# Kernel tuning notes

Measured on AMD Instinct MI355X. Metric: run time of the kernel, lower is better.

Reference implementation:

```python
import jax, jax.numpy as jnp
import numpy as np

N_EXPERTS = 8
TOP_K = 2

def setup_inputs() -> dict:
    key = jax.random.key(0)
    k1, k2, k3, k4 = jax.random.split(key, 4)
    B, T, C, F, E = 4, 1024, 1024, 2048, N_EXPERTS
    x = jax.random.normal(k1, (B, T, C), dtype=jnp.float32)
    router_w = jax.random.normal(k2, (E, C), dtype=jnp.float32) * 0.02
    w_v = jax.random.normal(k3, (E, C, 2 * F), dtype=jnp.float32) * 0.02
    c_proj = jax.random.normal(k4, (E, F, C), dtype=jnp.float32) * 0.02
    return {"x": x, "router_w": router_w, "w_v": w_v, "c_proj": c_proj}

def reference(x, router_w, w_v, c_proj):
    B, T, C = x.shape
    E = router_w.shape[0]
    # Router: top-k softmax
    logits = jnp.einsum('btc,ec->bte', x, router_w)
    probs = jax.nn.softmax(logits, axis=-1)
    weights, indices = jax.lax.top_k(probs, TOP_K)          # [B,T,K]
    weights = weights / jnp.sum(weights, axis=-1, keepdims=True)
    avg_probs = jnp.mean(probs, axis=(0, 1))
    aux_loss = E * jnp.sum(avg_probs * avg_probs)
    # Dense per-expert SwiGLU MLP on all tokens (idiomatic jax MoE reference)
    xf = x.reshape(B * T, C)                                # [N,C]
    h = jnp.einsum('nc,ecf->enf', xf, w_v)                  # [E,N,2F]
    gate, value = jnp.split(h, 2, axis=-1)
    act = jax.nn.silu(gate) * value                         # [E,N,F]
    eo = jnp.einsum('enf,efc->nec', act, c_proj)            # [N,E,C]
    # Combine: gather each token's top-k expert outputs and weight-sum
    idx = indices.reshape(B * T, TOP_K)                     # [N,K]
    w = weights.reshape(B * T, TOP_K)                       # [N,K]
    sel = jnp.take_along_axis(eo, idx[:, :, None], axis=1)  # [N,K,C]
    out = jnp.sum(w[:, :, None] * sel, axis=1)              # [N,C]
    return out.reshape(B, T, C), aux_loss
```

## Files before the change

kernel.cpp:

```cpp
#include <hip/hip_runtime.h>
#include <hip/hip_bf16.h>
#include <stdint.h>

#define N_TOK 4096
#define C_DIM 1024
#define F_DIM 2048
#define E_NUM 8
#define SMAX 9216
#define TILES_MAX 72
#define RBLK 1024

typedef __attribute__((ext_vector_type(4))) float f32x4;
typedef __attribute__((ext_vector_type(8))) short s16x8;

__device__ __forceinline__ uint16_t f2bf(float f) {
    unsigned x;
    __builtin_memcpy(&x, &f, 4);
    unsigned r = (x + 0x7fffu + ((x >> 16) & 1u)) >> 16;
    return (uint16_t)r;
}
__device__ __forceinline__ float bf2f(uint16_t u) {
    unsigned v = (unsigned)u << 16;
    float f;
    __builtin_memcpy(&f, &v, 4);
    return f;
}

#define GLL16(gp, lp)                                                                  \
    __builtin_amdgcn_global_load_lds((const __attribute__((address_space(1))) unsigned int*)(gp), \
                                     (__attribute__((address_space(3))) unsigned int*)(lp), 16, 0, 0)

__global__ void router_kernel(const float* __restrict__ x, const float* __restrict__ rw,
                              int* __restrict__ topk_idx, float* __restrict__ topk_w,
                              float* __restrict__ psum_part, int* __restrict__ cnt_part) {
    __shared__ float s_p[E_NUM];
    __shared__ int s_c[E_NUM];
    if (threadIdx.x < E_NUM) { s_p[threadIdx.x] = 0.f; s_c[threadIdx.x] = 0; }
    __syncthreads();

    int lane = threadIdx.x & 63;
    int wv = threadIdx.x >> 6;
    int t = blockIdx.x * 4 + wv;

    const float* xr = x + (size_t)t * C_DIM + lane * 16;
    float xs[16];
    for (int i = 0; i < 4; i++) *(float4*)&xs[i * 4] = *(const float4*)(xr + i * 4);

    float acc[E_NUM];
    for (int e = 0; e < E_NUM; e++) {
        const float* wr = rw + e * C_DIM + lane * 16;
        float s = 0.f;
        for (int i = 0; i < 4; i++) {
            float4 v = *(const float4*)(wr + i * 4);
            s += xs[i * 4] * v.x + xs[i * 4 + 1] * v.y + xs[i * 4 + 2] * v.z + xs[i * 4 + 3] * v.w;
        }
        acc[e] = s;
    }
    for (int off = 32; off > 0; off >>= 1)
        for (int e = 0; e < E_NUM; e++) acc[e] += __shfl_down(acc[e], off, 64);

    if (lane == 0) {
        float m = acc[0];
        for (int e = 1; e < E_NUM; e++) m = fmaxf(m, acc[e]);
        float p[E_NUM], s = 0.f;
        for (int e = 0; e < E_NUM; e++) { p[e] = __expf(acc[e] - m); s += p[e]; }
        float inv = 1.f / s;
        for (int e = 0; e < E_NUM; e++) { p[e] *= inv; atomicAdd(&s_p[e], p[e]); }
        int i0 = 0;
        for (int e = 1; e < E_NUM; e++) if (p[e] > p[i0]) i0 = e;
        int i1 = (i0 == 0) ? 1 : 0;
        for (int e = 0; e < E_NUM; e++) if (e != i0 && p[e] > p[i1]) i1 = e;
        float w0 = p[i0], w1 = p[i1], wsum = w0 + w1;
        topk_idx[t * 2] = i0; topk_idx[t * 2 + 1] = i1;
        topk_w[t * 2] = w0 / wsum; topk_w[t * 2 + 1] = w1 / wsum;
        atomicAdd(&s_c[i0], 1); atomicAdd(&s_c[i1], 1);
    }
    __syncthreads();
    if (threadIdx.x < E_NUM) {
        psum_part[blockIdx.x * E_NUM + threadIdx.x] = s_p[threadIdx.x];
        cnt_part[blockIdx.x * E_NUM + threadIdx.x] = s_c[threadIdx.x];
    }
}

__global__ void reduce_plan_kernel(const float* __restrict__ psum_part, const int* __restrict__ cnt_part,
                                   int* __restrict__ offsets, int* __restrict__ tile_expert,
                                   int* __restrict__ tile_row0, float* __restrict__ aux_out) {
    __shared__ float sp[256];
    __shared__ int sc[256];
    __shared__ int s_count[E_NUM];
    __shared__ float s_psum[E_NUM];
    int e = threadIdx.x >> 5, i = threadIdx.x & 31;
    float fp = 0.f; int c = 0;
    for (int j = i; j < RBLK; j += 32) { fp += psum_part[j * E_NUM + e]; c += cnt_part[j * E_NUM + e]; }
    sp[threadIdx.x] = fp; sc[threadIdx.x] = c;
    __syncthreads();
    for (int s = 16; s > 0; s >>= 1) {
        if (i < s) { sp[threadIdx.x] += sp[threadIdx.x + s]; sc[threadIdx.x] += sc[threadIdx.x + s]; }
        __syncthreads();
    }
    if (i == 0) { s_count[e] = sc[threadIdx.x]; s_psum[e] = sp[threadIdx.x]; }
    __syncthreads();
    if (threadIdx.x == 0) {
        int off = 0, t = 0;
        for (int ee = 0; ee < E_NUM; ee++) {
            offsets[ee] = off;
            int n = s_count[ee];
            int nt = (n + 127) >> 7;
            for (int k = 0; k < nt; k++) { tile_expert[t] = ee; tile_row0[t] = off + k * 128; t++; }
            off += nt * 128;
        }
        offsets[E_NUM] = off;
        for (; t < TILES_MAX; t++) tile_expert[t] = -1;
        float s = 0.f;
        for (int ee = 0; ee < E_NUM; ee++) { float a = s_psum[ee] * (1.f / N_TOK); s += a * a; }
        aux_out[0] = 8.f * s;
    }
}

__global__ void assign_kernel(const int* __restrict__ topk_idx, const float* __restrict__ topk_w,
                              const int* __restrict__ offsets, int* __restrict__ count2,
                              int* __restrict__ slot_map, float* __restrict__ slot_w,
                              int* __restrict__ tok_slot) {
    __shared__ int h[E_NUM];
    __shared__ int base[E_NUM];
    if (threadIdx.x < E_NUM) h[threadIdx.x] = 0;
    __syncthreads();
    int item = blockIdx.x * 256 + threadIdx.x;
    int e = topk_idx[item];
    int rank = atomicAdd(&h[e], 1);
    __syncthreads();
    if (threadIdx.x < E_NUM)
        base[threadIdx.x] = offsets[threadIdx.x] + atomicAdd(&count2[threadIdx.x], h[threadIdx.x]);
    __syncthreads();
    int slot = base[e] + rank;
    slot_map[slot] = item;
    slot_w[slot] = topk_w[item];
    tok_slot[item] = slot;
}

__global__ void gather_kernel(const float* __restrict__ x, const int* __restrict__ slot_map,
                              uint16_t* __restrict__ x_slots) {
    int slot = blockIdx.x;
    int item = slot_map[slot];
    if (item < 0) return;
    int t = item >> 1;
    float4 v = *(const float4*)(x + (size_t)t * C_DIM + threadIdx.x * 4);
    union { uint16_t u[4]; uint2 q; } r;
    r.u[0] = f2bf(v.x); r.u[1] = f2bf(v.y); r.u[2] = f2bf(v.z); r.u[3] = f2bf(v.w);
    *(uint2*)(x_slots + (size_t)slot * C_DIM + threadIdx.x * 4) = r.q;
}

__global__ __launch_bounds__(256) void convT_both(const float* __restrict__ wv, uint16_t* __restrict__ wvT,
                                                  const float* __restrict__ cp, uint16_t* __restrict__ cpT) {
    __shared__ uint16_t s[128 * 66];
    int bid = blockIdx.x;
    const float* in; uint16_t* out; int R, Cc, bx, by, bz;
    if (bid < 4096) {
        in = wv; out = wvT; R = 1024; Cc = 4096;
        bx = bid & 63; by = (bid >> 6) & 7; bz = bid >> 9;
    } else {
        int b = bid - 4096;
        in = cp; out = cpT; R = 2048; Cc = 1024;
        bx = b & 15; by = (b >> 4) & 15; bz = b >> 8;
    }
    size_t zb = (size_t)bz * (size_t)R * Cc;
    int c0 = bx * 64, r0 = by * 128;
    int cx = (threadIdx.x & 15) * 4, ry = threadIdx.x >> 4;
    for (int j = 0; j < 8; j++) {
        int r = ry + j * 16;
        float4 v = *(const float4*)(in + zb + (size_t)(r0 + r) * Cc + c0 + cx);
        uint16_t* p = &s[r * 66 + cx];
        p[0] = f2bf(v.x); p[1] = f2bf(v.y); p[2] = f2bf(v.z); p[3] = f2bf(v.w);
    }
    __syncthreads();
    int oc = threadIdx.x & 63, wseg = threadIdx.x >> 6;
    uint16_t tmp[32];
    for (int j = 0; j < 32; j++) tmp[j] = s[(wseg * 32 + j) * 66 + oc];
    uint4* dst = (uint4*)(out + zb + (size_t)(c0 + oc) * R + r0 + wseg * 32);
    dst[0] = *(const uint4*)&tmp[0];
    dst[1] = *(const uint4*)&tmp[8];
    dst[2] = *(const uint4*)&tmp[16];
    dst[3] = *(const uint4*)&tmp[24];
}


__global__ __launch_bounds__(256, 4) void gemm1_kernel(const uint16_t* __restrict__ x_slots,
                                                       const uint16_t* __restrict__ wvT,
                                                       const int* __restrict__ tile_expert,
                                                       const int* __restrict__ tile_row0,
                                                       uint16_t* __restrict__ act) {
    int e = tile_expert[blockIdx.y];
    if (e < 0) return;
    int row0 = tile_row0[blockIdx.y];
    int j = blockIdx.x;
    __shared__ uint16_t As[128 * 32];
    __shared__ uint16_t Bg[64 * 32];
    __shared__ uint16_t Bv[64 * 32];
    int lane = threadIdx.x & 63, w = threadIdx.x >> 6;
    int wm = w & 1, wn = w >> 1;
    const uint16_t* wvb = wvT + (size_t)e * 4096 * 1024;

    int sk = (((lane & 3) ^ ((lane >> 3) & 3))) * 8;
    int ar = w * 32 + (lane >> 2);
    const uint16_t* agp0 = x_slots + (size_t)(row0 + ar) * C_DIM + sk;
    const uint16_t* agp1 = agp0 + (size_t)16 * C_DIM;
    int br = w * 16 + (lane >> 2);
    const uint16_t* bgp = wvb + (size_t)(j * 64 + br) * C_DIM + sk;
    const uint16_t* bvp = wvb + (size_t)(2048 + j * 64 + br) * C_DIM + sk;

    int cswz = ((lane >> 4) ^ ((lane >> 1) & 3)) * 8;

    f32x4 accg[4][2], accv[4][2];
    f32x4 z4 = {0.f, 0.f, 0.f, 0.f};
    for (int mf = 0; mf < 4; mf++)
        for (int nf = 0; nf < 2; nf++) { accg[mf][nf] = z4; accv[mf][nf] = z4; }

    for (int kt = 0; kt < 32; ++kt) {
        int ko = kt * 32;
        __syncthreads();
        GLL16(agp0 + ko, As + w * 1024);
        GLL16(agp1 + ko, As + w * 1024 + 512);
        GLL16(bgp + ko, Bg + w * 512);
        GLL16(bvp + ko, Bv + w * 512);
        __syncthreads();
        s16x8 af[4], bg[2], bv[2];
        for (int mf = 0; mf < 4; mf++)
            af[mf] = *(const s16x8*)&As[(wm * 64 + mf * 16 + (lane & 15)) * 32 + cswz];
        for (int nf = 0; nf < 2; nf++) {
            bg[nf] = *(const s16x8*)&Bg[(wn * 32 + nf * 16 + (lane & 15)) * 32 + cswz];
            bv[nf] = *(const s16x8*)&Bv[(wn * 32 + nf * 16 + (lane & 15)) * 32 + cswz];
        }
        for (int mf = 0; mf < 4; mf++)
            for (int nf = 0; nf < 2; nf++) {
                accg[mf][nf] = __builtin_amdgcn_mfma_f32_16x16x32_bf16(af[mf], bg[nf], accg[mf][nf], 0, 0, 0);
                accv[mf][nf] = __builtin_amdgcn_mfma_f32_16x16x32_bf16(af[mf], bv[nf], accv[mf][nf], 0, 0, 0);
            }
    }
    for (int mf = 0; mf < 4; mf++)
        for (int nf = 0; nf < 2; nf++)
            for (int r = 0; r < 4; r++) {
                int row = row0 + wm * 64 + mf * 16 + (lane >> 4) * 4 + r;
                int col = j * 64 + wn * 32 + nf * 16 + (lane & 15);
                float g = accg[mf][nf][r], v = accv[mf][nf][r];
                float a = g * v / (1.f + __expf(-g));
                act[(size_t)row * F_DIM + col] = f2bf(a);
            }
}

__global__ __launch_bounds__(256) void gemm2_kernel(const uint16_t* __restrict__ act,
                                                    const uint16_t* __restrict__ cpT,
                                                    const int* __restrict__ tile_expert,
                                                    const int* __restrict__ tile_row0,
                                                    const int* __restrict__ slot_map,
                                                    const float* __restrict__ slot_w,
                                                    uint16_t* __restrict__ eo) {
    int e = tile_expert[blockIdx.y];
    if (e < 0) return;
    int row0 = tile_row0[blockIdx.y];
    int cb = blockIdx.x * 128;
    __shared__ uint16_t As[128 * 32];
    __shared__ uint16_t Bs[128 * 32];
    int lane = threadIdx.x & 63, w = threadIdx.x >> 6;
    int wm = w & 1, wn = w >> 1;
    const uint16_t* cpb = cpT + (size_t)e * 1024 * 2048;

    int sk = (((lane & 3) ^ ((lane >> 3) & 3))) * 8;
    int ar = w * 32 + (lane >> 2);
    const uint16_t* agp0 = act + (size_t)(row0 + ar) * F_DIM + sk;
    const uint16_t* agp1 = agp0 + (size_t)16 * F_DIM;
    const uint16_t* bgp0 = cpb + (size_t)(cb + ar) * F_DIM + sk;
    const uint16_t* bgp1 = bgp0 + (size_t)16 * F_DIM;

    int cswz = ((lane >> 4) ^ ((lane >> 1) & 3)) * 8;

    f32x4 acc[4][4];
    f32x4 z4 = {0.f, 0.f, 0.f, 0.f};
    for (int mf = 0; mf < 4; mf++)
        for (int nf = 0; nf < 4; nf++) acc[mf][nf] = z4;

    for (int kt = 0; kt < 64; ++kt) {
        int ko = kt * 32;
        __syncthreads();
        GLL16(agp0 + ko, As + w * 1024);
        GLL16(agp1 + ko, As + w * 1024 + 512);
        GLL16(bgp0 + ko, Bs + w * 1024);
        GLL16(bgp1 + ko, Bs + w * 1024 + 512);
        __syncthreads();
        s16x8 af[4], bf[4];
        for (int mf = 0; mf < 4; mf++)
            af[mf] = *(const s16x8*)&As[(wm * 64 + mf * 16 + (lane & 15)) * 32 + cswz];
        for (int nf = 0; nf < 4; nf++)
            bf[nf] = *(const s16x8*)&Bs[(wn * 64 + nf * 16 + (lane & 15)) * 32 + cswz];
        for (int mf = 0; mf < 4; mf++)
            for (int nf = 0; nf < 4; nf++)
                acc[mf][nf] = __builtin_amdgcn_mfma_f32_16x16x32_bf16(af[mf], bf[nf], acc[mf][nf], 0, 0, 0);
    }
    for (int mf = 0; mf < 4; mf++)
        for (int r = 0; r < 4; r++) {
            int slotr = row0 + wm * 64 + mf * 16 + (lane >> 4) * 4 + r;
            int t2k = slot_map[slotr];
            if (t2k < 0) continue;
            float wgt = slot_w[slotr];
            for (int nf = 0; nf < 4; nf++) {
                int col = cb + wn * 64 + nf * 16 + (lane & 15);
                eo[(size_t)slotr * C_DIM + col] = f2bf(wgt * acc[mf][nf][r]);
            }
        }
}

__global__ void combine_kernel(const uint16_t* __restrict__ eo, const int* __restrict__ tok_slot,
                               float* __restrict__ out) {
    int t = blockIdx.x;
    int s0 = tok_slot[2 * t], s1 = tok_slot[2 * t + 1];
    int c = threadIdx.x * 4;
    uint2 a = *(const uint2*)(eo + (size_t)s0 * C_DIM + c);
    uint2 b = *(const uint2*)(eo + (size_t)s1 * C_DIM + c);
    float4 o;
    o.x = bf2f((uint16_t)(a.x & 0xffff)) + bf2f((uint16_t)(b.x & 0xffff));
    o.y = bf2f((uint16_t)(a.x >> 16)) + bf2f((uint16_t)(b.x >> 16));
    o.z = bf2f((uint16_t)(a.y & 0xffff)) + bf2f((uint16_t)(b.y & 0xffff));
    o.w = bf2f((uint16_t)(a.y >> 16)) + bf2f((uint16_t)(b.y >> 16));
    *(float4*)(out + (size_t)t * C_DIM + c) = o;
}

extern "C" void kernel_launch(void* const* d_in, const int* in_sizes, int n_in,
                              void* d_out, int out_size, void* d_ws, size_t ws_size,
                              hipStream_t stream) {
    (void)in_sizes; (void)n_in; (void)out_size; (void)ws_size;
    const float* x = (const float*)d_in[0];
    const float* rw = (const float*)d_in[1];
    const float* wv = (const float*)d_in[2];
    const float* cp = (const float*)d_in[3];
    float* out = (float*)d_out;

    char* ws = (char*)d_ws;
    size_t off = 0;
    auto alloc = [&](size_t sz) -> void* {
        off = (off + 255) & ~(size_t)255;
        void* p = ws + off;
        off += sz;
        return p;
    };
    uint16_t* wvT = (uint16_t*)alloc((size_t)E_NUM * 4096 * 1024 * 2);
    uint16_t* cpT = (uint16_t*)alloc((size_t)E_NUM * 1024 * 2048 * 2);
    uint16_t* x_slots = (uint16_t*)alloc((size_t)SMAX * C_DIM * 2);
    uint16_t* act = (uint16_t*)alloc((size_t)SMAX * F_DIM * 2);
    uint16_t* eo = (uint16_t*)alloc((size_t)SMAX * C_DIM * 2);
    float* psum_part = (float*)alloc((size_t)RBLK * E_NUM * 4);
    int* cnt_part = (int*)alloc((size_t)RBLK * E_NUM * 4);
    int* count2 = (int*)alloc(E_NUM * 4);
    int* offsets = (int*)alloc((E_NUM + 1) * 4);
    int* tile_expert = (int*)alloc(TILES_MAX * 4);
    int* tile_row0 = (int*)alloc(TILES_MAX * 4);
    int* topk_idx = (int*)alloc((size_t)N_TOK * 2 * 4);
    float* topk_w = (float*)alloc((size_t)N_TOK * 2 * 4);
    int* slot_map = (int*)alloc((size_t)SMAX * 4);
    float* slot_w = (float*)alloc((size_t)SMAX * 4);
    int* tok_slot = (int*)alloc((size_t)N_TOK * 2 * 4);

    hipMemsetAsync(count2, 0, E_NUM * 4, stream);
    hipMemsetAsync(slot_map, 0xFF, (size_t)SMAX * 4, stream);

    router_kernel<<<RBLK, 256, 0, stream>>>(x, rw, topk_idx, topk_w, psum_part, cnt_part);
    reduce_plan_kernel<<<1, 256, 0, stream>>>(psum_part, cnt_part, offsets, tile_expert, tile_row0,
                                              out + (size_t)N_TOK * C_DIM);
    assign_kernel<<<N_TOK * 2 / 256, 256, 0, stream>>>(topk_idx, topk_w, offsets, count2,
                                                       slot_map, slot_w, tok_slot);
    gather_kernel<<<SMAX, 256, 0, stream>>>(x, slot_map, x_slots);
    convT_both<<<6144, 256, 0, stream>>>(wv, wvT, cp, cpT);
    gemm1_kernel<<<dim3(32, TILES_MAX), 256, 0, stream>>>(x_slots, wvT, tile_expert, tile_row0, act);
    gemm2_kernel<<<dim3(8, TILES_MAX), 256, 0, stream>>>(act, cpT, tile_expert, tile_row0,
                                                         slot_map, slot_w, eo);
    combine_kernel<<<N_TOK, 256, 0, stream>>>(eo, tok_slot, out);
}
```

Before: 481.3 us.

## Fuse combine into gemm2 via fp32 atomics and double K-step in gemm1

Removes the bf16 expert-output buffer and the combine kernel. gemm2 now scatters weighted results straight into the zeroed fp32 output using atomicAdd, after a memset of the output. Separately, gemm1 loads two 32-wide K slices per barrier pair, which halves the number of syncs per K loop at the cost of twice the LDS per block. The atomics add contention and make the summation order nondeterministic, and the larger LDS footprint may lower occupancy in gemm1.

Measured after the change: 488.9 us. About the same (+1.6%).

```diff
diff --git a/kernel.cpp b/kernel.cpp
--- a/kernel.cpp
+++ b/kernel.cpp
@@ -119,8 +119,7 @@
 
 __global__ void assign_kernel(const int* __restrict__ topk_idx, const float* __restrict__ topk_w,
                               const int* __restrict__ offsets, int* __restrict__ count2,
-                              int* __restrict__ slot_map, float* __restrict__ slot_w,
-                              int* __restrict__ tok_slot) {
+                              int* __restrict__ slot_map, float* __restrict__ slot_w) {
     __shared__ int h[E_NUM];
     __shared__ int base[E_NUM];
     if (threadIdx.x < E_NUM) h[threadIdx.x] = 0;
@@ -135,7 +134,6 @@
     int slot = base[e] + rank;
     slot_map[slot] = item;
     slot_w[slot] = topk_w[item];
-    tok_slot[item] = slot;
 }
 
 __global__ void gather_kernel(const float* __restrict__ x, const int* __restrict__ slot_map,
@@ -193,9 +191,9 @@
     if (e < 0) return;
     int row0 = tile_row0[blockIdx.y];
     int j = blockIdx.x;
-    __shared__ uint16_t As[128 * 32];
-    __shared__ uint16_t Bg[64 * 32];
-    __shared__ uint16_t Bv[64 * 32];
+    __shared__ uint16_t As[2][128 * 32];
+    __shared__ uint16_t Bg[2][64 * 32];
+    __shared__ uint16_t Bv[2][64 * 32];
     int lane = threadIdx.x & 63, w = threadIdx.x >> 6;
     int wm = w & 1, wn = w >> 1;
     const uint16_t* wvb = wvT + (size_t)e * 4096 * 1024;
@@ -215,26 +213,32 @@
     for (int mf = 0; mf < 4; mf++)
         for (int nf = 0; nf < 2; nf++) { accg[mf][nf] = z4; accv[mf][nf] = z4; }
 
-    for (int kt = 0; kt < 32; ++kt) {
-        int ko = kt * 32;
-        __syncthreads();
-        GLL16(agp0 + ko, As + w * 1024);
-        GLL16(agp1 + ko, As + w * 1024 + 512);
-        GLL16(bgp + ko, Bg + w * 512);
-        GLL16(bvp + ko, Bv + w * 512);
-        __syncthreads();
-        s16x8 af[4], bg[2], bv[2];
-        for (int mf = 0; mf < 4; mf++)
-            af[mf] = *(const s16x8*)&As[(wm * 64 + mf * 16 + (lane & 15)) * 32 + cswz];
-        for (int nf = 0; nf < 2; nf++) {
-            bg[nf] = *(const s16x8*)&Bg[(wn * 32 + nf * 16 + (lane & 15)) * 32 + cswz];
-            bv[nf] = *(const s16x8*)&Bv[(wn * 32 + nf * 16 + (lane & 15)) * 32 + cswz];
-        }
-        for (int mf = 0; mf < 4; mf++)
+    for (int kt = 0; kt < 16; ++kt) {
+        int ko = kt * 64;
+        __syncthreads();
+#pragma unroll
+        for (int kk = 0; kk < 2; kk++) {
+            GLL16(agp0 + ko + kk * 32, As[kk] + w * 1024);
+            GLL16(agp1 + ko + kk * 32, As[kk] + w * 1024 + 512);
+            GLL16(bgp + ko + kk * 32, Bg[kk] + w * 512);
+            GLL16(bvp + ko + kk * 32, Bv[kk] + w * 512);
+        }
+        __syncthreads();
+#pragma unroll
+        for (int kk = 0; kk < 2; kk++) {
+            s16x8 af[4], bg[2], bv[2];
+            for (int mf = 0; mf < 4; mf++)
+                af[mf] = *(const s16x8*)&As[kk][(wm * 64 + mf * 16 + (lane & 15)) * 32 + cswz];
             for (int nf = 0; nf < 2; nf++) {
-                accg[mf][nf] = __builtin_amdgcn_mfma_f32_16x16x32_bf16(af[mf], bg[nf], accg[mf][nf], 0, 0, 0);
-                accv[mf][nf] = __builtin_amdgcn_mfma_f32_16x16x32_bf16(af[mf], bv[nf], accv[mf][nf], 0, 0, 0);
+                bg[nf] = *(const s16x8*)&Bg[kk][(wn * 32 + nf * 16 + (lane & 15)) * 32 + cswz];
+                bv[nf] = *(const s16x8*)&Bv[kk][(wn * 32 + nf * 16 + (lane & 15)) * 32 + cswz];
             }
+            for (int mf = 0; mf < 4; mf++)
+                for (int nf = 0; nf < 2; nf++) {
+                    accg[mf][nf] = __builtin_amdgcn_mfma_f32_16x16x32_bf16(af[mf], bg[nf], accg[mf][nf], 0, 0, 0);
+                    accv[mf][nf] = __builtin_amdgcn_mfma_f32_16x16x32_bf16(af[mf], bv[nf], accv[mf][nf], 0, 0, 0);
+                }
+        }
     }
     for (int mf = 0; mf < 4; mf++)
         for (int nf = 0; nf < 2; nf++)
@@ -253,7 +257,7 @@
                                                     const int* __restrict__ tile_row0,
                                                     const int* __restrict__ slot_map,
                                                     const float* __restrict__ slot_w,
-                                                    uint16_t* __restrict__ eo) {
+                                                    float* __restrict__ out) {
     int e = tile_expert[blockIdx.y];
     if (e < 0) return;
     int row0 = tile_row0[blockIdx.y];
@@ -298,29 +302,15 @@
     for (int mf = 0; mf < 4; mf++)
         for (int r = 0; r < 4; r++) {
             int slotr = row0 + wm * 64 + mf * 16 + (lane >> 4) * 4 + r;
-            int t2k = slot_map[slotr];
-            if (t2k < 0) continue;
+            int item = slot_map[slotr];
+            if (item < 0) continue;
+            int tok = item >> 1;
             float wgt = slot_w[slotr];
             for (int nf = 0; nf < 4; nf++) {
                 int col = cb + wn * 64 + nf * 16 + (lane & 15);
-                eo[(size_t)slotr * C_DIM + col] = f2bf(wgt * acc[mf][nf][r]);
+                atomicAdd(&out[(size_t)tok * C_DIM + col], wgt * acc[mf][nf][r]);
             }
         }
-}
-
-__global__ void combine_kernel(const uint16_t* __restrict__ eo, const int* __restrict__ tok_slot,
-                               float* __restrict__ out) {
-    int t = blockIdx.x;
-    int s0 = tok_slot[2 * t], s1 = tok_slot[2 * t + 1];
-    int c = threadIdx.x * 4;
-    uint2 a = *(const uint2*)(eo + (size_t)s0 * C_DIM + c);
-    uint2 b = *(const uint2*)(eo + (size_t)s1 * C_DIM + c);
-    float4 o;
-    o.x = bf2f((uint16_t)(a.x & 0xffff)) + bf2f((uint16_t)(b.x & 0xffff));
-    o.y = bf2f((uint16_t)(a.x >> 16)) + bf2f((uint16_t)(b.x >> 16));
-    o.z = bf2f((uint16_t)(a.y & 0xffff)) + bf2f((uint16_t)(b.y & 0xffff));
-    o.w = bf2f((uint16_t)(a.y >> 16)) + bf2f((uint16_t)(b.y >> 16));
-    *(float4*)(out + (size_t)t * C_DIM + c) = o;
 }
 
 extern "C" void kernel_launch(void* const* d_in, const int* in_sizes, int n_in,
@@ -345,7 +335,6 @@
     uint16_t* cpT = (uint16_t*)alloc((size_t)E_NUM * 1024 * 2048 * 2);
     uint16_t* x_slots = (uint16_t*)alloc((size_t)SMAX * C_DIM * 2);
     uint16_t* act = (uint16_t*)alloc((size_t)SMAX * F_DIM * 2);
-    uint16_t* eo = (uint16_t*)alloc((size_t)SMAX * C_DIM * 2);
     float* psum_part = (float*)alloc((size_t)RBLK * E_NUM * 4);
     int* cnt_part = (int*)alloc((size_t)RBLK * E_NUM * 4);
     int* count2 = (int*)alloc(E_NUM * 4);
@@ -356,20 +345,19 @@
     float* topk_w = (float*)alloc((size_t)N_TOK * 2 * 4);
     int* slot_map = (int*)alloc((size_t)SMAX * 4);
     float* slot_w = (float*)alloc((size_t)SMAX * 4);
-    int* tok_slot = (int*)alloc((size_t)N_TOK * 2 * 4);
 
     hipMemsetAsync(count2, 0, E_NUM * 4, stream);
     hipMemsetAsync(slot_map, 0xFF, (size_t)SMAX * 4, stream);
+    hipMemsetAsync(out, 0, (size_t)N_TOK * C_DIM * 4, stream);
 
     router_kernel<<<RBLK, 256, 0, stream>>>(x, rw, topk_idx, topk_w, psum_part, cnt_part);
     reduce_plan_kernel<<<1, 256, 0, stream>>>(psum_part, cnt_part, offsets, tile_expert, tile_row0,
                                               out + (size_t)N_TOK * C_DIM);
     assign_kernel<<<N_TOK * 2 / 256, 256, 0, stream>>>(topk_idx, topk_w, offsets, count2,
-                                                       slot_map, slot_w, tok_slot);
+                                                       slot_map, slot_w);
     gather_kernel<<<SMAX, 256, 0, stream>>>(x, slot_map, x_slots);
     convT_both<<<6144, 256, 0, stream>>>(wv, wvT, cp, cpT);
     gemm1_kernel<<<dim3(32, TILES_MAX), 256, 0, stream>>>(x_slots, wvT, tile_expert, tile_row0, act);
     gemm2_kernel<<<dim3(8, TILES_MAX), 256, 0, stream>>>(act, cpT, tile_expert, tile_row0,
-                                                         slot_map, slot_w, eo);
-    combine_kernel<<<N_TOK, 256, 0, stream>>>(eo, tok_slot, out);
-}
+                                                         slot_map, slot_w, out);
+}
```
